# Performance work log

Hardware: AMD Instinct MI355X
Metric: run time of the kernel (lower is better)

## Reference

```python
import jax, jax.numpy as jnp
import numpy as np

B, T, L, R, E, F = 8, 16, 128, 1024, 5, 512
# range(min_dist_exp, max_dist_exp+1) with 0 removed, per Diffusion.__init__
DIST_EXPONENTS = jnp.array([-3.0, -2.0, -1.0, 1.0, 2.0], dtype=jnp.float32)


def setup_inputs() -> dict:
    key = jax.random.key(0)
    ks = jax.random.split(key, 8)
    return {
        "lig_feat": jax.random.normal(ks[0], (B, L, E, F), jnp.float32) * 0.1,
        "rec_feat": jax.random.normal(ks[1], (B, R, E, F), jnp.float32) * 0.1,
        # coords on ~angstrom scale so negative-power distances stay bounded
        "lig_coord": jax.random.normal(ks[2], (B, L, 3), jnp.float32) * 5.0,
        "rec_coord": jax.random.normal(ks[3], (B, R, 3), jnp.float32) * 5.0,
        "pre_rot": jax.random.normal(ks[4], (B, T, 3, 3), jnp.float32),
        "trans": jax.random.normal(ks[5], (B, T, 3), jnp.float32),
        "lig_counts": jax.random.randint(ks[6], (B,), L // 2, L + 1, jnp.int32),
        "rec_counts": jax.random.randint(ks[7], (B,), R // 2, R + 1, jnp.int32),
    }


def reference(lig_feat, rec_feat, lig_coord, rec_coord, pre_rot, trans,
              lig_counts, rec_counts):
    # get_energy over a ragged batch (padded + masked), vectorized over
    # graphs (b) and timesteps (t). rot = QR(pre_rot) as in energy_grad.
    exps = DIST_EXPONENTS.astype(lig_feat.dtype)          # [E]
    rot = jnp.linalg.qr(pre_rot)[0]                       # [B,T,3,3]
    # einsum('nij,bj->nbi', rot, lig_coord) + trans, batched over graphs
    new_lig = jnp.einsum('btij,blj->btli', rot, lig_coord) + trans[:, :, None, :]  # [B,T,L,3]

    lig_mask = jnp.arange(lig_coord.shape[1]) < lig_counts[:, None]   # [B,L]
    rec_mask = jnp.arange(rec_coord.shape[1]) < rec_counts[:, None]   # [B,R]
    pair_mask = lig_mask[:, :, None] & rec_mask[:, None, :]           # [B,L,R]

    # atn_coefs = einsum('lef,ref->lre'); zero out padded pairs
    atn = jnp.einsum('blef,bref->blre', lig_feat, rec_feat) * pair_mask[..., None]  # [B,L,R,E]

    diff = new_lig[:, :, :, None, :] - rec_coord[:, None, None, :, :]  # [B,T,L,R,3]
    dists = jnp.sqrt(jnp.sum(diff * diff, axis=-1))                    # [B,T,L,R]
    # padded pairs -> 1.0 so negative exponents don't produce inf*0
    dists = jnp.where(pair_mask[:, None, :, :], dists, 1.0)
    dist_exp = dists[..., None] ** exps                                # [B,T,L,R,E]

    U = jnp.einsum('blre,btlre->bt', atn, dist_exp)                    # [B,T]
    return U
```

## Files before the change

kernel.cpp:

```cpp
#include <hip/hip_runtime.h>

#define B_ 8
#define T_ 16
#define L_ 128
#define R_ 1024
#define E_ 5
#define F_ 512

typedef short short8 __attribute__((ext_vector_type(8)));
typedef float floatx4 __attribute__((ext_vector_type(4)));

__device__ __forceinline__ unsigned short f2bf(float f) {
  unsigned u = __float_as_uint(f);
  return (unsigned short)((u + 0x8000u) >> 16);
}

__device__ __forceinline__ short8 pack8(floatx4 lo, floatx4 hi) {
  short8 v;
  v[0] = (short)f2bf(lo[0]); v[1] = (short)f2bf(lo[1]);
  v[2] = (short)f2bf(lo[2]); v[3] = (short)f2bf(lo[3]);
  v[4] = (short)f2bf(hi[0]); v[5] = (short)f2bf(hi[1]);
  v[6] = (short)f2bf(hi[2]); v[7] = (short)f2bf(hi[3]);
  return v;
}

__device__ __forceinline__ void stage16(const float* g, float* lds) {
  __builtin_amdgcn_global_load_lds(
      (const __attribute__((address_space(1))) void*)g,
      (__attribute__((address_space(3))) void*)lds, 16, 0, 0);
}

#define WAITCNT_VM6 0xF76
#define WAITCNT_VM0 0xF70

__global__ void prep_kernel(const float* __restrict__ lig_coord,
                            const float* __restrict__ pre_rot,
                            const float* __restrict__ trans,
                            float* __restrict__ new_lig,
                            float* __restrict__ out) {
  int bt = blockIdx.x;
  __shared__ float Qs[3][3];
  if (threadIdx.x == 0) {
    out[bt] = 0.f;
    float a[3][3], q[3][3];
    #pragma unroll
    for (int i = 0; i < 3; ++i)
      #pragma unroll
      for (int j = 0; j < 3; ++j) {
        a[i][j] = pre_rot[(bt * 3 + i) * 3 + j];
        q[i][j] = (i == j) ? 1.f : 0.f;
      }
    for (int k = 0; k < 3; ++k) {
      float alpha = a[k][k];
      float xn2 = 0.f;
      for (int i = k + 1; i < 3; ++i) xn2 += a[i][k] * a[i][k];
      float nrm = sqrtf(alpha * alpha + xn2);
      if (xn2 > 0.f && nrm > 0.f) {
        float beta = (alpha >= 0.f) ? -nrm : nrm;
        float tau = (beta - alpha) / beta;
        float inv = 1.f / (alpha - beta);
        float v[3] = {0.f, 0.f, 0.f};
        v[k] = 1.f;
        for (int i = k + 1; i < 3; ++i) v[i] = a[i][k] * inv;
        for (int j = k; j < 3; ++j) {
          float w = 0.f;
          for (int i = k; i < 3; ++i) w += v[i] * a[i][j];
          w *= tau;
          for (int i = k; i < 3; ++i) a[i][j] -= w * v[i];
        }
        for (int i = 0; i < 3; ++i) {
          float w = 0.f;
          for (int j = k; j < 3; ++j) w += q[i][j] * v[j];
          w *= tau;
          for (int j = k; j < 3; ++j) q[i][j] -= w * v[j];
        }
      }
    }
    for (int i = 0; i < 3; ++i)
      for (int j = 0; j < 3; ++j) Qs[i][j] = q[i][j];
  }
  __syncthreads();
  int b = bt >> 4;
  int l = threadIdx.x;
  float cx = lig_coord[(b * L_ + l) * 3 + 0];
  float cy = lig_coord[(b * L_ + l) * 3 + 1];
  float cz = lig_coord[(b * L_ + l) * 3 + 2];
  float nx = Qs[0][0] * cx + Qs[0][1] * cy + Qs[0][2] * cz + trans[bt * 3 + 0];
  float ny = Qs[1][0] * cx + Qs[1][1] * cy + Qs[1][2] * cz + trans[bt * 3 + 1];
  float nz = Qs[2][0] * cx + Qs[2][1] * cy + Qs[2][2] * cz + trans[bt * 3 + 2];
  float* o = new_lig + ((size_t)bt * L_ + l) * 3;
  o[0] = nx; o[1] = ny; o[2] = nz;
}

template <int EIDX>
__device__ __forceinline__ void phaseB(const floatx4 (&acc)[2][4],
                                       const float* nlp,
                                       const float (&rcx)[4],
                                       const float (&rcy)[4],
                                       const float (&rcz)[4],
                                       int wm, int quad, int lane, int wave,
                                       float (*smr)[T_]) {
  #pragma unroll 1
  for (int tg = 0; tg < 4; ++tg) {
    #pragma unroll
    for (int it = 0; it < 4; ++it) {
      const int t = tg * 4 + it;
      float uacc = 0.f;
      #pragma unroll
      for (int i = 0; i < 2; ++i)
        #pragma unroll
        for (int reg = 0; reg < 4; ++reg) {
          const int m = wm + i * 16 + quad * 4 + reg;
          const float* np = nlp + (t * L_ + m) * 3;
          const float nx = np[0], ny = np[1], nz = np[2];
          #pragma unroll
          for (int j = 0; j < 4; ++j) {
            float dx = nx - rcx[j];
            float dy = ny - rcy[j];
            float dz = nz - rcz[j];
            float d2 = fmaf(dx, dx, fmaf(dy, dy, dz * dz));
            d2 = fmaxf(d2, 1e-20f);
            float p;
            if constexpr (EIDX == 0) {
              float rs = rsqrtf(d2); p = rs * rs * rs;
            } else if constexpr (EIDX == 1) {
              float rs = rsqrtf(d2); p = rs * rs;
            } else if constexpr (EIDX == 2) {
              p = rsqrtf(d2);
            } else if constexpr (EIDX == 3) {
              float rs = rsqrtf(d2); p = d2 * rs;
            } else {
              p = d2;
            }
            uacc = fmaf(acc[i][j][reg], p, uacc);
          }
        }
      #pragma unroll
      for (int m_ = 32; m_ > 0; m_ >>= 1) uacc += __shfl_xor(uacc, m_, 64);
      if (lane == 0) smr[wave][t] = uacc;
    }
    __syncthreads();
  }
}

__launch_bounds__(256)
__global__ void fused_kernel(const float* __restrict__ lig_feat,
                             const float* __restrict__ rec_feat,
                             const float* __restrict__ rec_coord,
                             const int* __restrict__ lig_counts,
                             const int* __restrict__ rec_counts,
                             const float* __restrict__ new_lig,
                             float* __restrict__ out) {
  const int rt = blockIdx.x;
  const int e  = blockIdx.y;
  const int b  = blockIdx.z;
  const int r0 = rt * 64;
  const int recN = rec_counts[b];
  if (r0 >= recN) return;

  __shared__ __align__(16) float As[2][128 * 32];
  __shared__ __align__(16) float Bs[2][64 * 32];
  __shared__ float smr[4][T_];

  const int tid  = threadIdx.x;
  const int wave = tid >> 6;
  const int lane = tid & 63;
  const int lrow = lane & 15;
  const int quad = lane >> 4;
  const int wm   = wave * 32;

  const int lr8 = lane >> 3;
  const int sw  = (lane & 7) ^ lr8;
  const float* ga[4];
  #pragma unroll
  for (int i = 0; i < 4; ++i) {
    int row = wave * 32 + i * 8 + lr8;
    ga[i] = lig_feat + ((size_t)(b * L_ + row) * E_ + e) * F_ + sw * 4;
  }
  const float* gb[2];
  #pragma unroll
  for (int i = 0; i < 2; ++i) {
    int row = wave * 16 + i * 8 + lr8;
    gb[i] = rec_feat + ((size_t)(b * R_ + r0 + row) * E_ + e) * F_ + sw * 4;
  }

  floatx4 acc[2][4];
  #pragma unroll
  for (int i = 0; i < 2; ++i)
    #pragma unroll
    for (int j = 0; j < 4; ++j)
      acc[i][j] = (floatx4){0.f, 0.f, 0.f, 0.f};

  const int c0 = (2 * quad) ^ (lane & 7);

  #pragma unroll
  for (int i = 0; i < 4; ++i) stage16(ga[i], &As[0][(wave * 32 + i * 8) * 32]);
  #pragma unroll
  for (int i = 0; i < 2; ++i) stage16(gb[i], &Bs[0][(wave * 16 + i * 8) * 32]);

  #pragma unroll 1
  for (int kc = 0; kc < 16; ++kc) {
    const int cur = kc & 1;
    if (kc > 0)
      __builtin_amdgcn_s_barrier();
    if (kc < 15) {
      const int col = (kc + 1) * 32;
      #pragma unroll
      for (int i = 0; i < 4; ++i)
        stage16(ga[i] + col, &As[cur ^ 1][(wave * 32 + i * 8) * 32]);
      #pragma unroll
      for (int i = 0; i < 2; ++i)
        stage16(gb[i] + col, &Bs[cur ^ 1][(wave * 16 + i * 8) * 32]);
      __builtin_amdgcn_s_waitcnt(WAITCNT_VM6);
    } else {
      __builtin_amdgcn_s_waitcnt(WAITCNT_VM0);
    }
    __builtin_amdgcn_s_barrier();
    __builtin_amdgcn_sched_barrier(0);

    short8 af[2], bfv[4];
    #pragma unroll
    for (int i = 0; i < 2; ++i) {
      const float* base = &As[cur][(wm + i * 16 + lrow) * 32];
      af[i] = pack8(*(const floatx4*)(base + c0 * 4),
                    *(const floatx4*)(base + (c0 ^ 1) * 4));
    }
    #pragma unroll
    for (int j = 0; j < 4; ++j) {
      const float* base = &Bs[cur][(j * 16 + lrow) * 32];
      bfv[j] = pack8(*(const floatx4*)(base + c0 * 4),
                     *(const floatx4*)(base + (c0 ^ 1) * 4));
    }
    #pragma unroll
    for (int i = 0; i < 2; ++i)
      #pragma unroll
      for (int j = 0; j < 4; ++j)
        acc[i][j] = __builtin_amdgcn_mfma_f32_16x16x32_bf16(af[i], bfv[j], acc[i][j], 0, 0, 0);
  }

  __syncthreads();


  float* const nlp = &As[0][0];
  {
    const floatx4* src = (const floatx4*)(new_lig + (size_t)b * T_ * L_ * 3);
    floatx4* dst = (floatx4*)nlp;
    #pragma unroll
    for (int i = 0; i < 6; ++i) dst[tid + i * 256] = src[tid + i * 256];
  }
  __syncthreads();

  const int ligN = lig_counts[b];
  #pragma unroll
  for (int j = 0; j < 4; ++j) {
    const bool nv = (r0 + j * 16 + lrow) < recN;
    #pragma unroll
    for (int i = 0; i < 2; ++i)
      #pragma unroll
      for (int reg = 0; reg < 4; ++reg) {
        const bool mv = (wm + i * 16 + quad * 4 + reg) < ligN;
        if (!(nv && mv)) acc[i][j][reg] = 0.f;
      }
  }

  float rcx[4], rcy[4], rcz[4];
  #pragma unroll
  for (int j = 0; j < 4; ++j) {
    const float* rp = rec_coord + (size_t)(b * R_ + r0 + j * 16 + lrow) * 3;
    rcx[j] = rp[0]; rcy[j] = rp[1]; rcz[j] = rp[2];
  }

  if (e == 0)      phaseB<0>(acc, nlp, rcx, rcy, rcz, wm, quad, lane, wave, smr);
  else if (e == 1) phaseB<1>(acc, nlp, rcx, rcy, rcz, wm, quad, lane, wave, smr);
  else if (e == 2) phaseB<2>(acc, nlp, rcx, rcy, rcz, wm, quad, lane, wave, smr);
  else if (e == 3) phaseB<3>(acc, nlp, rcx, rcy, rcz, wm, quad, lane, wave, smr);
  else             phaseB<4>(acc, nlp, rcx, rcy, rcz, wm, quad, lane, wave, smr);

  __syncthreads();
  if (tid < T_) {
    float s = smr[0][tid] + smr[1][tid] + smr[2][tid] + smr[3][tid];
    atomicAdd(&out[b * T_ + tid], s);
  }
}

extern "C" void kernel_launch(void* const* d_in, const int* in_sizes, int n_in,
                              void* d_out, int out_size, void* d_ws, size_t ws_size,
                              hipStream_t stream) {
  const float* lig_feat   = (const float*)d_in[0];
  const float* rec_feat   = (const float*)d_in[1];
  const float* lig_coord  = (const float*)d_in[2];
  const float* rec_coord  = (const float*)d_in[3];
  const float* pre_rot    = (const float*)d_in[4];
  const float* trans      = (const float*)d_in[5];
  const int*   lig_counts = (const int*)d_in[6];
  const int*   rec_counts = (const int*)d_in[7];
  float* out = (float*)d_out;

  float* new_lig = (float*)d_ws;

  prep_kernel<<<dim3(B_ * T_), dim3(L_), 0, stream>>>(lig_coord, pre_rot, trans,
                                                      new_lig, out);
  fused_kernel<<<dim3(R_ / 64, E_, B_), dim3(256), 0, stream>>>(
      lig_feat, rec_feat, rec_coord, lig_counts, rec_counts, new_lig, out);
}
```

Before: 180.5 us.

## Load GEMM fragments directly from global into registers, drop LDS staging

Replaces the double-buffered global-to-LDS staging of the lig/rec feature tiles with direct per-lane global loads into registers, software-pipelined two chunks ahead, removing all barriers in the k-loop. The new_lig copy into shared memory now happens before the GEMM, so it overlaps with the feature loads, and shared memory shrinks to just the coordinate buffer, which may help occupancy. It also removes the per-timestep __syncthreads inside phaseB. Trade-offs: each lane now issues uncoalesced 32-byte row-strided loads, B fragments are re-read by all four waves instead of being shared through LDS, and register pressure rises from the prefetched fragments.

New measurement: 200.7 us. 1.11x slower.

```diff
diff --git a/kernel.cpp b/kernel.cpp
--- a/kernel.cpp
+++ b/kernel.cpp
@@ -24,14 +24,13 @@
   return v;
 }
 
-__device__ __forceinline__ void stage16(const float* g, float* lds) {
-  __builtin_amdgcn_global_load_lds(
-      (const __attribute__((address_space(1))) void*)g,
-      (__attribute__((address_space(3))) void*)lds, 16, 0, 0);
-}
-
-#define WAITCNT_VM6 0xF76
-#define WAITCNT_VM0 0xF70
+struct Frag { floatx4 lo, hi; };
+__device__ __forceinline__ Frag ldfrag(const float* __restrict__ p) {
+  Frag f;
+  f.lo = *(const floatx4*)p;
+  f.hi = *(const floatx4*)(p + 4);
+  return f;
+}
 
 __global__ void prep_kernel(const float* __restrict__ lig_coord,
                             const float* __restrict__ pre_rot,
@@ -139,7 +138,6 @@
       for (int m_ = 32; m_ > 0; m_ >>= 1) uacc += __shfl_xor(uacc, m_, 64);
       if (lane == 0) smr[wave][t] = uacc;
     }
-    __syncthreads();
   }
 }
 
@@ -158,8 +156,7 @@
   const int recN = rec_counts[b];
   if (r0 >= recN) return;
 
-  __shared__ __align__(16) float As[2][128 * 32];
-  __shared__ __align__(16) float Bs[2][64 * 32];
+  __shared__ __align__(16) float nls[T_ * L_ * 3];
   __shared__ float smr[4][T_];
 
   const int tid  = threadIdx.x;
@@ -169,20 +166,19 @@
   const int quad = lane >> 4;
   const int wm   = wave * 32;
 
-  const int lr8 = lane >> 3;
-  const int sw  = (lane & 7) ^ lr8;
-  const float* ga[4];
-  #pragma unroll
-  for (int i = 0; i < 4; ++i) {
-    int row = wave * 32 + i * 8 + lr8;
-    ga[i] = lig_feat + ((size_t)(b * L_ + row) * E_ + e) * F_ + sw * 4;
-  }
-  const float* gb[2];
-  #pragma unroll
-  for (int i = 0; i < 2; ++i) {
-    int row = wave * 16 + i * 8 + lr8;
-    gb[i] = rec_feat + ((size_t)(b * R_ + r0 + row) * E_ + e) * F_ + sw * 4;
-  }
+  {
+    const floatx4* src = (const floatx4*)(new_lig + (size_t)b * T_ * L_ * 3);
+    floatx4* dst = (floatx4*)nls;
+    #pragma unroll
+    for (int i = 0; i < 6; ++i) dst[tid + i * 256] = src[tid + i * 256];
+  }
+
+  const float* pA0 = lig_feat + ((size_t)(b * L_ + wm + 0  + lrow) * E_ + e) * F_ + quad * 8;
+  const float* pA1 = lig_feat + ((size_t)(b * L_ + wm + 16 + lrow) * E_ + e) * F_ + quad * 8;
+  const float* pB0 = rec_feat + ((size_t)(b * R_ + r0 + 0  + lrow) * E_ + e) * F_ + quad * 8;
+  const float* pB1 = rec_feat + ((size_t)(b * R_ + r0 + 16 + lrow) * E_ + e) * F_ + quad * 8;
+  const float* pB2 = rec_feat + ((size_t)(b * R_ + r0 + 32 + lrow) * E_ + e) * F_ + quad * 8;
+  const float* pB3 = rec_feat + ((size_t)(b * R_ + r0 + 48 + lrow) * E_ + e) * F_ + quad * 8;
 
   floatx4 acc[2][4];
   #pragma unroll
@@ -191,64 +187,60 @@
     for (int j = 0; j < 4; ++j)
       acc[i][j] = (floatx4){0.f, 0.f, 0.f, 0.f};
 
-  const int c0 = (2 * quad) ^ (lane & 7);
-
-  #pragma unroll
-  for (int i = 0; i < 4; ++i) stage16(ga[i], &As[0][(wave * 32 + i * 8) * 32]);
-  #pragma unroll
-  for (int i = 0; i < 2; ++i) stage16(gb[i], &Bs[0][(wave * 16 + i * 8) * 32]);
+  Frag A0a = ldfrag(pA0), A1a = ldfrag(pA1);
+  Frag B0a = ldfrag(pB0), B1a = ldfrag(pB1), B2a = ldfrag(pB2), B3a = ldfrag(pB3);
 
   #pragma unroll 1
-  for (int kc = 0; kc < 16; ++kc) {
-    const int cur = kc & 1;
-    if (kc > 0)
-      __builtin_amdgcn_s_barrier();
-    if (kc < 15) {
-      const int col = (kc + 1) * 32;
-      #pragma unroll
-      for (int i = 0; i < 4; ++i)
-        stage16(ga[i] + col, &As[cur ^ 1][(wave * 32 + i * 8) * 32]);
-      #pragma unroll
-      for (int i = 0; i < 2; ++i)
-        stage16(gb[i] + col, &Bs[cur ^ 1][(wave * 16 + i * 8) * 32]);
-      __builtin_amdgcn_s_waitcnt(WAITCNT_VM6);
-    } else {
-      __builtin_amdgcn_s_waitcnt(WAITCNT_VM0);
-    }
-    __builtin_amdgcn_s_barrier();
-    __builtin_amdgcn_sched_barrier(0);
-
-    short8 af[2], bfv[4];
-    #pragma unroll
-    for (int i = 0; i < 2; ++i) {
-      const float* base = &As[cur][(wm + i * 16 + lrow) * 32];
-      af[i] = pack8(*(const floatx4*)(base + c0 * 4),
-                    *(const floatx4*)(base + (c0 ^ 1) * 4));
-    }
-    #pragma unroll
-    for (int j = 0; j < 4; ++j) {
-      const float* base = &Bs[cur][(j * 16 + lrow) * 32];
-      bfv[j] = pack8(*(const floatx4*)(base + c0 * 4),
-                     *(const floatx4*)(base + (c0 ^ 1) * 4));
-    }
-    #pragma unroll
-    for (int i = 0; i < 2; ++i)
-      #pragma unroll
-      for (int j = 0; j < 4; ++j)
-        acc[i][j] = __builtin_amdgcn_mfma_f32_16x16x32_bf16(af[i], bfv[j], acc[i][j], 0, 0, 0);
+  for (int kc = 0; kc < 16; kc += 2) {
+    const int o1 = (kc + 1) * 32;
+    Frag A0b = ldfrag(pA0 + o1), A1b = ldfrag(pA1 + o1);
+    Frag B0b = ldfrag(pB0 + o1), B1b = ldfrag(pB1 + o1);
+    Frag B2b = ldfrag(pB2 + o1), B3b = ldfrag(pB3 + o1);
+
+    {
+      short8 af0 = pack8(A0a.lo, A0a.hi);
+      short8 af1 = pack8(A1a.lo, A1a.hi);
+      short8 bf0 = pack8(B0a.lo, B0a.hi);
+      short8 bf1 = pack8(B1a.lo, B1a.hi);
+      short8 bf2 = pack8(B2a.lo, B2a.hi);
+      short8 bf3 = pack8(B3a.lo, B3a.hi);
+      acc[0][0] = __builtin_amdgcn_mfma_f32_16x16x32_bf16(af0, bf0, acc[0][0], 0, 0, 0);
+      acc[0][1] = __builtin_amdgcn_mfma_f32_16x16x32_bf16(af0, bf1, acc[0][1], 0, 0, 0);
+      acc[0][2] = __builtin_amdgcn_mfma_f32_16x16x32_bf16(af0, bf2, acc[0][2], 0, 0, 0);
+      acc[0][3] = __builtin_amdgcn_mfma_f32_16x16x32_bf16(af0, bf3, acc[0][3], 0, 0, 0);
+      acc[1][0] = __builtin_amdgcn_mfma_f32_16x16x32_bf16(af1, bf0, acc[1][0], 0, 0, 0);
+      acc[1][1] = __builtin_amdgcn_mfma_f32_16x16x32_bf16(af1, bf1, acc[1][1], 0, 0, 0);
+      acc[1][2] = __builtin_amdgcn_mfma_f32_16x16x32_bf16(af1, bf2, acc[1][2], 0, 0, 0);
+      acc[1][3] = __builtin_amdgcn_mfma_f32_16x16x32_bf16(af1, bf3, acc[1][3], 0, 0, 0);
+    }
+
+    if (kc + 2 < 16) {
+      const int o2 = (kc + 2) * 32;
+      A0a = ldfrag(pA0 + o2); A1a = ldfrag(pA1 + o2);
+      B0a = ldfrag(pB0 + o2); B1a = ldfrag(pB1 + o2);
+      B2a = ldfrag(pB2 + o2); B3a = ldfrag(pB3 + o2);
+    }
+
+    {
+      short8 af0 = pack8(A0b.lo, A0b.hi);
+      short8 af1 = pack8(A1b.lo, A1b.hi);
+      short8 bf0 = pack8(B0b.lo, B0b.hi);
+      short8 bf1 = pack8(B1b.lo, B1b.hi);
+      short8 bf2 = pack8(B2b.lo, B2b.hi);
+      short8 bf3 = pack8(B3b.lo, B3b.hi);
+      acc[0][0] = __builtin_amdgcn_mfma_f32_16x16x32_bf16(af0, bf0, acc[0][0], 0, 0, 0);
+      acc[0][1] = __builtin_amdgcn_mfma_f32_16x16x32_bf16(af0, bf1, acc[0][1], 0, 0, 0);
+      acc[0][2] = __builtin_amdgcn_mfma_f32_16x16x32_bf16(af0, bf2, acc[0][2], 0, 0, 0);
+      acc[0][3] = __builtin_amdgcn_mfma_f32_16x16x32_bf16(af0, bf3, acc[0][3], 0, 0, 0);
+      acc[1][0] = __builtin_amdgcn_mfma_f32_16x16x32_bf16(af1, bf0, acc[1][0], 0, 0, 0);
+      acc[1][1] = __builtin_amdgcn_mfma_f32_16x16x32_bf16(af1, bf1, acc[1][1], 0, 0, 0);
+      acc[1][2] = __builtin_amdgcn_mfma_f32_16x16x32_bf16(af1, bf2, acc[1][2], 0, 0, 0);
+      acc[1][3] = __builtin_amdgcn_mfma_f32_16x16x32_bf16(af1, bf3, acc[1][3], 0, 0, 0);
+    }
   }
 
   __syncthreads();
 
-
-  float* const nlp = &As[0][0];
-  {
-    const floatx4* src = (const floatx4*)(new_lig + (size_t)b * T_ * L_ * 3);
-    floatx4* dst = (floatx4*)nlp;
-    #pragma unroll
-    for (int i = 0; i < 6; ++i) dst[tid + i * 256] = src[tid + i * 256];
-  }
-  __syncthreads();
 
   const int ligN = lig_counts[b];
   #pragma unroll
@@ -270,11 +262,11 @@
     rcx[j] = rp[0]; rcy[j] = rp[1]; rcz[j] = rp[2];
   }
 
-  if (e == 0)      phaseB<0>(acc, nlp, rcx, rcy, rcz, wm, quad, lane, wave, smr);
-  else if (e == 1) phaseB<1>(acc, nlp, rcx, rcy, rcz, wm, quad, lane, wave, smr);
-  else if (e == 2) phaseB<2>(acc, nlp, rcx, rcy, rcz, wm, quad, lane, wave, smr);
-  else if (e == 3) phaseB<3>(acc, nlp, rcx, rcy, rcz, wm, quad, lane, wave, smr);
-  else             phaseB<4>(acc, nlp, rcx, rcy, rcz, wm, quad, lane, wave, smr);
+  if (e == 0)      phaseB<0>(acc, nls, rcx, rcy, rcz, wm, quad, lane, wave, smr);
+  else if (e == 1) phaseB<1>(acc, nls, rcx, rcy, rcz, wm, quad, lane, wave, smr);
+  else if (e == 2) phaseB<2>(acc, nls, rcx, rcy, rcz, wm, quad, lane, wave, smr);
+  else if (e == 3) phaseB<3>(acc, nls, rcx, rcy, rcz, wm, quad, lane, wave, smr);
+  else             phaseB<4>(acc, nls, rcx, rcy, rcz, wm, quad, lane, wave, smr);
 
   __syncthreads();
   if (tid < T_) {
```
